# Optimization experiments

Hardware: AMD Instinct MI355X
Metric: run time of the kernel (lower is better)

## Reference

```python
import jax, jax.numpy as jnp
import numpy as np

TAU = 2.0        # LIFNode tau
ALPHA = 4.0      # spikingjelly default Sigmoid surrogate alpha
SCALE = 0.125    # attention scale from SSA
EPS = 1e-5       # BatchNorm eps

@jax.custom_vjp
def heaviside(x):
    return (x >= 0).astype(x.dtype)

def _hv_fwd(x):
    return (x >= 0).astype(x.dtype), x

def _hv_bwd(x, g):
    s = jax.nn.sigmoid(ALPHA * x)
    return (g * ALPHA * s * (1.0 - s),)

heaviside.defvjp(_hv_fwd, _hv_bwd)

def lif(x_seq, v_th):
    """Multi-step LIF (decay_input=True, v_reset=0, hard reset, detach_reset=True).
    x_seq: (T, ...) -> spikes (T, ...)."""
    def step(v, x):
        h = v + (x - v) / TAU                      # membrane charge
        s = heaviside(h - v_th)                    # spike
        v_new = h * (1.0 - jax.lax.stop_gradient(s))  # detached hard reset to 0
        return v_new, s
    _, spikes = jax.lax.scan(step, jnp.zeros_like(x_seq[0]), x_seq)
    return spikes

def conv_bn(x, w, gamma, beta, mean, var):
    """3x3 same-pad conv (no bias) + BatchNorm2d (eval: running stats), applied over merged T*B."""
    T, B, C, H, W = x.shape
    y = jax.lax.conv_general_dilated(
        x.reshape(T * B, C, H, W), w, (1, 1), 'SAME',
        dimension_numbers=('NCHW', 'OIHW', 'NCHW'))
    scale = gamma / jnp.sqrt(var + EPS)
    y = y * scale[:, None, None] + (beta - mean * scale)[:, None, None]
    return y.reshape(T, B, C, H, W)

def setup_inputs() -> dict:
    key = jax.random.key(0)
    T, B, C, H, W = 4, 16, 768, 16, 16
    ks = jax.random.split(key, 5)
    d = {"x": jax.random.normal(ks[0], (T, B, C, H, W), jnp.float32)}
    for i, p in enumerate(["q", "k", "v", "p"]):
        kk = jax.random.split(ks[i + 1], 5)
        d[p + "_w"] = jax.random.normal(kk[0], (C, C, 3, 3), jnp.float32) * 0.02
        d[p + "_gamma"] = jax.random.uniform(kk[1], (C,), jnp.float32, 0.5, 1.5)
        d[p + "_beta"] = jax.random.normal(kk[2], (C,), jnp.float32) * 0.1
        d[p + "_mean"] = jax.random.normal(kk[3], (C,), jnp.float32) * 0.1
        d[p + "_var"] = jax.random.uniform(kk[4], (C,), jnp.float32, 0.5, 1.5)
    return d

def reference(x, q_w, q_gamma, q_beta, q_mean, q_var,
              k_w, k_gamma, k_beta, k_mean, k_var,
              v_w, v_gamma, v_beta, v_mean, v_var,
              p_w, p_gamma, p_beta, p_mean, p_var):
    T, B, C, H, W = x.shape
    N = H * W
    nh = 8
    dh = C // nh
    xs = lif(x, 1.0)                                   # head_lif
    # Scaler is identity in eval mode (and rate=1.0)
    q = lif(conv_bn(xs, q_w, q_gamma, q_beta, q_mean, q_var), 1.0)
    k = lif(conv_bn(xs, k_w, k_gamma, k_beta, k_mean, k_var), 1.0)
    v = lif(conv_bn(xs, v_w, v_gamma, v_beta, v_mean, v_var), 1.0)
    def to_heads(t):  # (T,B,C,H,W) -> (T,B,nh,N,dh)
        return t.reshape(T, B, C, N).transpose(0, 1, 3, 2).reshape(T, B, N, nh, dh).transpose(0, 1, 3, 2, 4)
    q, k, v = to_heads(q), to_heads(k), to_heads(v)
    kv = jnp.einsum('tbhnd,tbhne->tbhde', k, v)        # k^T @ v (linear attention)
    o = jnp.einsum('tbhnd,tbhde->tbhne', q, kv) * SCALE
    o = o.transpose(0, 1, 2, 4, 3).reshape(T, B, C, N)  # (T,B,h,d,N) -> (T,B,C,N)
    o = lif(o, 0.5).reshape(T, B, C, H, W)              # attn_lif with v_threshold=0.5
    return conv_bn(o, p_w, p_gamma, p_beta, p_mean, p_var)
```

## Files before the change

### kernel.cpp

```cpp
#include <hip/hip_runtime.h>

typedef __attribute__((ext_vector_type(4))) int   i32x4;
typedef __attribute__((ext_vector_type(4))) float f32x4;
typedef unsigned int u32;
typedef unsigned long long u64;
typedef unsigned char u8;
typedef unsigned short u16;

#define C_ 768
#define NPIX 256
#define ROWB 96
#define IMGBITS (324*ROWB)
#define GS   304
#define PRS  1232
#define AEXP_SZ 12320

#define WFRAG_SZ 10616832ull
#define OFF_WFRAG 0ull
#define OFF_WCOL  31850496ull
#define OFF_YBUF  42467328ull
#define OFF_BITS  92798976ull
#define BITSZ     1990656ull
#define OFF_SBT   102752256ull
#define OFF_WMAX  102776832ull

__device__ __forceinline__ i32x4 as_i4(uint4 v){ union{uint4 u; i32x4 s;} c; c.u=v; return c.s; }
#define SPREAD(NIB) ((u32)__mul24((int)(NIB), 0x204081) & 0x01010101u)

__global__ __launch_bounds__(256) void bn_prep4(
    const float* __restrict__ g0, const float* __restrict__ b0,
    const float* __restrict__ m0, const float* __restrict__ v0,
    const float* __restrict__ g1, const float* __restrict__ b1,
    const float* __restrict__ m1, const float* __restrict__ v1,
    const float* __restrict__ g2, const float* __restrict__ b2,
    const float* __restrict__ m2, const float* __restrict__ v2,
    const float* __restrict__ g3, const float* __restrict__ b3,
    const float* __restrict__ m3, const float* __restrict__ v3,
    float* __restrict__ out)
{
    int s = blockIdx.y;
    const float* g  = s==0?g0:s==1?g1:s==2?g2:g3;
    const float* be = s==0?b0:s==1?b1:s==2?b2:b3;
    const float* m  = s==0?m0:s==1?m1:s==2?m2:m3;
    const float* va = s==0?v0:s==1?v1:s==2?v2:v3;
    int i = blockIdx.x*256 + threadIdx.x;
    if (i < C_){
        float sc = g[i] / sqrtf(va[i] + 1e-5f);
        out[s*1536 + i] = sc;
        out[s*1536 + C_ + i] = be[i] - m[i]*sc;
    }
}

__global__ __launch_bounds__(256) void wmax4(
    const float* __restrict__ w0, const float* __restrict__ w1,
    const float* __restrict__ w2, const float* __restrict__ w3,
    float* __restrict__ out)
{
    int s = blockIdx.y;
    const float* w = s==0?w0:s==1?w1:s==2?w2:w3;
    const int n4 = 9*C_*C_/4;
    float m = 0.f;
    for (int i = blockIdx.x*256 + threadIdx.x; i < n4; i += 65536){
        f32x4 v = *(const f32x4*)(w + (size_t)i*4);
        m = fmaxf(m, fmaxf(fmaxf(fabsf(v[0]), fabsf(v[1])),
                           fmaxf(fabsf(v[2]), fabsf(v[3]))));
    }
    #pragma unroll
    for (int off = 32; off >= 1; off >>= 1)
        m = fmaxf(m, __shfl_xor(m, off));
    if ((threadIdx.x & 63) == 0)
        atomicMax((int*)(out + s), __float_as_int(m));
}

__global__ __launch_bounds__(256) void wprep_stage(
    const float* __restrict__ w0, const float* __restrict__ w1,
    const float* __restrict__ w2, const float* __restrict__ w3,
    const float* __restrict__ wmaxb, u8* __restrict__ wfbase,
    short* __restrict__ wcol)
{
    __shared__ float lds[16][580];
    const int tid = threadIdx.x;
    const int nfg = blockIdx.x, cch = blockIdx.y, s = blockIdx.z;
    const float* w = s==0?w0:s==1?w1:s==2?w2:w3;
    const float mw = wmaxb[s];
    const float invS = (mw > 0.f) ? (32512.0f / mw) : 0.f;

    #pragma unroll 1
    for (int i = tid; i < 16*144; i += 256){
        int r = i / 144, f4 = i - r*144;
        f32x4 v = *(const f32x4*)(w + (size_t)(nfg*16 + r)*6912 + cch*576 + f4*4);
        *(f32x4*)&lds[r][f4*4] = v;
    }
    __syncthreads();

    if (s < 3){
        u8* wf = wfbase + (size_t)s*WFRAG_SZ;
        #pragma unroll 1
        for (int rep = 0; rep < 3; ++rep){
            int idx = rep*256 + tid;
            if (idx < 576){
                int tap = idx >> 6, lane = idx & 63;
                int co_r = lane & 15, cg = lane >> 4;
                u32 hw[4] = {0,0,0,0}, lw[4] = {0,0,0,0};
                #pragma unroll
                for (int e=0;e<16;++e){
                    float f = lds[co_r][(cg*16 + e)*9 + tap];
                    int w16 = __float2int_rn(f * invS);
                    w16 = min(max(w16, -32512), 32512);
                    int hi = (w16 + 128) >> 8;
                    int lo = w16 - (hi << 8);
                    hw[e>>2] |= ((u32)(hi & 0xFF)) << ((e&3)*8);
                    lw[e>>2] |= ((u32)(lo & 0xFF)) << ((e&3)*8);
                }
                u8* base = wf + (((size_t)(cch*9 + tap)*48 + nfg)*2)*1024 + (size_t)lane*16;
                *(uint4*)(base)        = make_uint4(hw[0],hw[1],hw[2],hw[3]);
                *(uint4*)(base + 1024) = make_uint4(lw[0],lw[1],lw[2],lw[3]);
            }
        }
    } else {
        #pragma unroll 1
        for (int rep = 0; rep < 3; ++rep){
            int idx = rep*256 + tid;
            if (idx < 576){
                int tap = idx >> 6, cl = idx & 63;
                short ov[16];
                #pragma unroll
                for (int r=0;r<16;++r){
                    float f = lds[r][cl*9 + tap];
                    int w16 = __float2int_rn(f * invS);
                    w16 = min(max(w16, -32512), 32512);
                    ov[r] = (short)w16;
                }
                short* dst = wcol + ((size_t)tap*C_ + cch*64 + cl)*C_ + nfg*16;
                *(uint4*)(dst)     = *(uint4*)(&ov[0]);
                *(uint4*)(dst + 8) = *(uint4*)(&ov[8]);
            }
        }
    }
}

__global__ __launch_bounds__(256) void head_bits(
    const float* __restrict__ x, u8* __restrict__ bits)
{
    int gid = blockIdx.x*256 + threadIdx.x;
    int b = gid / 24576, rem = gid - b*24576;
    int cb = rem >> 8, pix = rem & 255;
    int pr = ((pix>>4)+1)*18 + (pix&15) + 1;
    float v[8];
    #pragma unroll
    for (int j=0;j<8;++j) v[j]=0.f;
    #pragma unroll
    for (int t=0;t<4;++t){
        int img = t*16 + b;
        u32 byte = 0;
        #pragma unroll
        for (int j=0;j<8;++j){
            float xv = x[((size_t)img*C_ + cb*8 + j)*NPIX + pix];
            float h = __fadd_rn(v[j], __fmul_rn(__fsub_rn(xv, v[j]), 0.5f));
            u32 s = (h >= 1.0f) ? 1u : 0u;
            v[j] = s ? 0.f : h;
            byte |= s << j;
        }
        bits[(size_t)img*IMGBITS + (size_t)pr*ROWB + cb] = (u8)byte;
    }
}

__global__ __launch_bounds__(256,2) void conv_i8(
    const u8* __restrict__ abits, const u8* __restrict__ wf,
    const float* __restrict__ sb, const float* __restrict__ wmaxp,
    float* __restrict__ ybuf)
{
    __shared__ __align__(16) u8 Aexp[2*AEXP_SZ];
    const int tid = threadIdx.x;
    const int bid = blockIdx.x;
    const int cox = bid & 7, mh = (bid >> 3) & 1, img = bid >> 4;
    const int lane = tid & 63, w = tid >> 6;
    const int wr = w >> 1, wc = w & 1;
    const int lrow = lane & 15, lgrp = lane >> 4;

    const int erow = (tid < 180) ? tid : 179;
    const int epr = erow / 18, epc = erow - epr*18;
    u8* edst = Aexp + epr*PRS + epc*16;
    const u8* bsrc = abits + (size_t)img*IMGBITS + (size_t)(mh*144)*ROWB;

#define EXPW(BW, BOFF) if (tid < 180){ \
    u8* dp = edst + (BOFF); \
    u32 lo_ = (u32)(BW), hi_ = (u32)((BW)>>32); \
    *(uint4*)(dp       ) = make_uint4(SPREAD(lo_&0xF), SPREAD((lo_>>4)&0xF), SPREAD((lo_>>8)&0xF), SPREAD((lo_>>12)&0xF)); \
    *(uint4*)(dp + GS  ) = make_uint4(SPREAD((lo_>>16)&0xF), SPREAD((lo_>>20)&0xF), SPREAD((lo_>>24)&0xF), SPREAD((lo_>>28)&0xF)); \
    *(uint4*)(dp + 2*GS) = make_uint4(SPREAD(hi_&0xF), SPREAD((hi_>>4)&0xF), SPREAD((hi_>>8)&0xF), SPREAD((hi_>>12)&0xF)); \
    *(uint4*)(dp + 3*GS) = make_uint4(SPREAD((hi_>>16)&0xF), SPREAD((hi_>>20)&0xF), SPREAD((hi_>>24)&0xF), SPREAD((hi_>>28)&0xF)); }

    const u8* wp = wf + (size_t)((cox*6 + wc*3)*2)*1024 + (size_t)lane*16;
    uint4 R0[6], R1[6], R2[6];
#define LOADB(BUF) { \
    _Pragma("unroll") \
    for (int j=0;j<6;++j) BUF[j] = *(const uint4*)(wp + (j>>1)*2048 + (j&1)*1024); \
    wp += 98304; }

    int rb[4];
    #pragma unroll
    for (int mi=0;mi<4;++mi)
        rb[mi] = (wr*4 + mi + 1)*PRS + lgrp*GS + (lrow+1)*16;

    i32x4 acc_h[4][3], acc_l[4][3];
    #pragma unroll
    for (int mi=0;mi<4;++mi)
        #pragma unroll
        for (int ni=0;ni<3;++ni)
            #pragma unroll
            for (int r=0;r<4;++r){ acc_h[mi][ni][r]=0; acc_l[mi][ni][r]=0; }

#define COMPUTE(BUF, AE, TAP) { \
    const int DT = ((TAP)/3 - 1)*PRS + (((TAP)%3) - 1)*16; \
    i32x4 af[4]; \
    _Pragma("unroll") \
    for (int mi=0;mi<4;++mi) af[mi] = *(const i32x4*)((AE) + rb[mi] + DT); \
    __builtin_amdgcn_s_setprio(1); \
    _Pragma("unroll") \
    for (int mi=0;mi<4;++mi){ \
        _Pragma("unroll") \
        for (int ni=0;ni<3;++ni){ \
            acc_h[mi][ni] = __builtin_amdgcn_mfma_i32_16x16x64_i8(af[mi], as_i4(BUF[ni*2+0]), acc_h[mi][ni], 0,0,0); \
            acc_l[mi][ni] = __builtin_amdgcn_mfma_i32_16x16x64_i8(af[mi], as_i4(BUF[ni*2+1]), acc_l[mi][ni], 0,0,0); \
        } \
    } \
    __builtin_amdgcn_s_setprio(0); }

#define BODY(CCH, BOFF) { \
    u64 bwn = 0; \
    if ((CCH) < 11) bwn = *(const u64*)(bsrc + erow*ROWB + ((CCH)+1)*8); \
    const u8* Ae = Aexp + (BOFF); \
    LOADB(R2); COMPUTE(R0, Ae, 0); \
    LOADB(R0); COMPUTE(R1, Ae, 1); \
    LOADB(R1); COMPUTE(R2, Ae, 2); \
    LOADB(R2); COMPUTE(R0, Ae, 3); \
    LOADB(R0); COMPUTE(R1, Ae, 4); \
    LOADB(R1); COMPUTE(R2, Ae, 5); \
    LOADB(R2); COMPUTE(R0, Ae, 6); \
    LOADB(R0); COMPUTE(R1, Ae, 7); \
    LOADB(R1); COMPUTE(R2, Ae, 8); \
    if ((CCH) < 11) EXPW(bwn, (BOFF) ^ AEXP_SZ); \
    __syncthreads(); }

    LOADB(R0); LOADB(R1);
    {
        u64 bw0 = *(const u64*)(bsrc + erow*ROWB);
        EXPW(bw0, 0);
    }
    __syncthreads();

    #pragma unroll 1
    for (int c2=0; c2<6; ++c2){
        BODY(2*c2,   0);
        BODY(2*c2+1, AEXP_SZ);
    }
#undef LOADB
#undef EXPW
#undef COMPUTE
#undef BODY

    const float S = (*wmaxp) * (1.0f/32512.0f);
    #pragma unroll
    for (int mi=0;mi<4;++mi){
        const int prow = mh*128 + wr*64 + mi*16 + lgrp*4;
        #pragma unroll
        for (int ni=0;ni<3;++ni){
            const int co = cox*96 + wc*48 + ni*16 + lrow;
            const float sc = sb[co], bi = sb[C_ + co];
            #pragma unroll
            for (int r=0;r<4;++r){
                float accf = (float)(acc_h[mi][ni][r]*256 + acc_l[mi][ni][r]) * S;
                ybuf[((size_t)img*NPIX + prow + r)*C_ + co] =
                    __fadd_rn(__fmul_rn(accf, sc), bi);
            }
        }
    }
}

__global__ __launch_bounds__(256) void lif_bits(
    const float* __restrict__ y, u8* __restrict__ bits)
{
    int gid = blockIdx.x*256 + threadIdx.x;
    int b = gid / 24576, rem = gid - b*24576;
    int pix = rem / 96, cb = rem - pix*96;
    int pr = ((pix>>4)+1)*18 + (pix&15) + 1;
    float v[8];
    #pragma unroll
    for (int j=0;j<8;++j) v[j]=0.f;
    #pragma unroll
    for (int t=0;t<4;++t){
        int img = t*16 + b;
        const float* yp = y + ((size_t)img*NPIX + pix)*C_ + cb*8;
        f32x4 y0 = *(const f32x4*)yp;
        f32x4 y1 = *(const f32x4*)(yp + 4);
        u32 byte = 0;
        #pragma unroll
        for (int j=0;j<8;++j){
            float yv = (j<4) ? y0[j] : y1[j-4];
            float h = __fadd_rn(v[j], __fmul_rn(__fsub_rn(yv, v[j]), 0.5f));
            u32 s = (h >= 1.0f) ? 1u : 0u;
            v[j] = s ? 0.f : h;
            byte |= s << j;
        }
        bits[(size_t)img*IMGBITS + (size_t)pr*ROWB + cb] = (u8)byte;
    }
}

__global__ __launch_bounds__(512) void attn_bits(
    const u8* __restrict__ qb_, const u8* __restrict__ kb_,
    const u8* __restrict__ vb_, u8* __restrict__ ob)
{
    const int tid = threadIdx.x;
    const int b = blockIdx.x, h = blockIdx.y;
    __shared__ u64 kb[96][4], vb[96][4];
    __shared__ float kvl[96][96];
    const int w = tid >> 6, lane = tid & 63;
    const int ng = w & 3, n_build = ng*64 + lane;
    const int n = tid & 255, eh = tid >> 8;
    const int prb = ((n_build>>4)+1)*18 + (n_build&15) + 1;
    const int prn = ((n>>4)+1)*18 + (n&15) + 1;
    float vmem[48];
    #pragma unroll
    for (int e=0;e<48;++e) vmem[e]=0.f;

    for (int t=0;t<4;++t){
        const int img = t*16 + b;
        {
            const u8* src = (w < 4 ? kb_ : vb_) + (size_t)img*IMGBITS
                          + (size_t)prb*ROWB + h*12;
            u32 kw0 = ((const u32*)src)[0];
            u32 kw1 = ((const u32*)src)[1];
            u32 kw2 = ((const u32*)src)[2];
            u64 (*dst)[4] = (w < 4) ? kb : vb;
            #pragma unroll 1
            for (int dj=0; dj<32; ++dj){
                u64 m = __ballot((int)((kw0 >> dj) & 1u));
                if (lane == 0) dst[dj][ng] = m;
            }
            #pragma unroll 1
            for (int dj=0; dj<32; ++dj){
                u64 m = __ballot((int)((kw1 >> dj) & 1u));
                if (lane == 0) dst[32+dj][ng] = m;
            }
            #pragma unroll 1
            for (int dj=0; dj<32; ++dj){
                u64 m = __ballot((int)((kw2 >> dj) & 1u));
                if (lane == 0) dst[64+dj][ng] = m;
            }
        }
        __syncthreads();
        for (int i = tid; i < 96*96; i += 512){
            int d = i / 96, e = i - d*96;
            int s = 0;
            #pragma unroll
            for (int g=0; g<4; ++g) s += __popcll(kb[d][g] & vb[e][g]);
            kvl[d][e] = (float)s;
        }
        __syncthreads();
        {
            const u8* qsrc = qb_ + (size_t)img*IMGBITS + (size_t)prn*ROWB + h*12;
            u32 qw0 = ((const u32*)qsrc)[0];
            u32 qw1 = ((const u32*)qsrc)[1];
            u32 qw2 = ((const u32*)qsrc)[2];
            float val[48];
            #pragma unroll
            for (int e=0;e<48;++e) val[e]=0.f;
            #pragma unroll 1
            for (int d=0; d<96; ++d){
                u32 ww = (d < 32) ? qw0 : (d < 64) ? qw1 : qw2;
                u32 qv = (ww >> (d & 31)) & 1u;
                if (__any((int)qv)){
                    float qf = (float)qv;
                    #pragma unroll
                    for (int e=0;e<48;++e) val[e] += qf * kvl[d][eh*48+e];
                }
            }
            u64 wbits = 0;
            #pragma unroll
            for (int e=0;e<48;++e){
                float o = val[e]*0.125f;
                float hh = __fadd_rn(vmem[e], __fmul_rn(__fsub_rn(o, vmem[e]), 0.5f));
                u32 s = (hh >= 0.5f) ? 1u : 0u;
                vmem[e] = s ? 0.f : hh;
                wbits |= (u64)s << e;
            }
            u8* od = ob + (size_t)img*IMGBITS + (size_t)prn*ROWB + h*12 + eh*6;
            *(u16*)(od)     = (u16)(wbits);
            *(u16*)(od + 2) = (u16)(wbits >> 16);
            *(u16*)(od + 4) = (u16)(wbits >> 32);
        }
        __syncthreads();
    }
}

__global__ __launch_bounds__(256) void pconv_sparse(
    const u8* __restrict__ ob, const short* __restrict__ wcol,
    const float* __restrict__ sb, const float* __restrict__ wmaxp,
    float* __restrict__ out)
{
    __shared__ u64 bl[648];
    __shared__ int accL[16*768];
    const int tid = threadIdx.x;
    const int img = blockIdx.x >> 4, y = blockIdx.x & 15;

    for (int idx = tid; idx < 648; idx += 256){
        int d = idx / 216, wi = idx - d*216;
        bl[idx] = *(const u64*)(ob + (size_t)img*IMGBITS
                                + (size_t)((y+d)*18)*ROWB + (size_t)wi*8);
    }
    for (int idx = tid; idx < 16*768; idx += 256) accL[idx] = 0;
    __syncthreads();

    #pragma unroll 1
    for (int wi = 0; wi < 648; ++wi){
        u64 v = bl[wi];
        if (!v) continue;
        while (v){
            int j = __ffsll((unsigned long long)v) - 1;
            v &= v - 1;
            int byt = wi*8 + (j >> 3);
            int p = byt / 96;
            int c = (byt - p*96)*8 + (j & 7);
            int dd = p / 18, px = p - dd*18;
            #pragma unroll
            for (int xi = 0; xi < 3; ++xi){
                int x = px - 2 + xi;
                if ((unsigned)x < 16u){
                    int tap = dd*3 + 2 - xi;
                    const short* wr_ = wcol + ((size_t)tap*C_ + c)*C_;
                    #pragma unroll
                    for (int q = 0; q < 3; ++q){
                        int co = tid + q*256;
                        accL[x*768 + co] += (int)wr_[co];
                    }
                }
            }
        }
    }
    __syncthreads();

    const float S = wmaxp[0] * (1.0f/32512.0f);
    #pragma unroll
    for (int q = 0; q < 3; ++q){
        int co = tid + q*256;
        float sc = sb[co], bi = sb[C_ + co];
        float* op = out + ((size_t)img*C_ + co)*NPIX + y*16;
        #pragma unroll
        for (int xg = 0; xg < 4; ++xg){
            f32x4 o4;
            #pragma unroll
            for (int rr = 0; rr < 4; ++rr){
                float accf = (float)accL[(xg*4+rr)*768 + co] * S;
                o4[rr] = __fadd_rn(__fmul_rn(accf, sc), bi);
            }
            *(f32x4*)(op + xg*4) = o4;
        }
    }
}

extern "C" void kernel_launch(void* const* d_in, const int* in_sizes, int n_in,
                              void* d_out, int out_size, void* d_ws, size_t ws_size,
                              hipStream_t stream)
{
    u8* ws = (u8*)d_ws;
    u8* wfrag = ws + OFF_WFRAG;
    short* wcol = (short*)(ws + OFF_WCOL);
    float* ybuf = (float*)(ws + OFF_YBUF);
    u8* xs_b = ws + OFF_BITS;
    u8* q_b  = ws + OFF_BITS + 1*BITSZ;
    u8* k_b  = ws + OFF_BITS + 2*BITSZ;
    u8* v_b  = ws + OFF_BITS + 3*BITSZ;
    u8* o_b  = ws + OFF_BITS + 4*BITSZ;
    float* sbt = (float*)(ws + OFF_SBT);
    float* wmaxb = (float*)(ws + OFF_WMAX);
    float* outp = (float*)d_out;

    hipMemsetAsync(ws + OFF_BITS, 0, 5*BITSZ, stream);
    hipMemsetAsync(wmaxb, 0, 16, stream);

    bn_prep4<<<dim3(3,4),256,0,stream>>>(
        (const float*)d_in[2],  (const float*)d_in[3],  (const float*)d_in[4],  (const float*)d_in[5],
        (const float*)d_in[7],  (const float*)d_in[8],  (const float*)d_in[9],  (const float*)d_in[10],
        (const float*)d_in[12], (const float*)d_in[13], (const float*)d_in[14], (const float*)d_in[15],
        (const float*)d_in[17], (const float*)d_in[18], (const float*)d_in[19], (const float*)d_in[20],
        sbt);
    wmax4<<<dim3(256,4),256,0,stream>>>(
        (const float*)d_in[1], (const float*)d_in[6],
        (const float*)d_in[11], (const float*)d_in[16], wmaxb);
    wprep_stage<<<dim3(48,12,4),256,0,stream>>>(
        (const float*)d_in[1], (const float*)d_in[6],
        (const float*)d_in[11], (const float*)d_in[16], wmaxb, wfrag, wcol);
    head_bits<<<1536,256,0,stream>>>((const float*)d_in[0], xs_b);

    u8* bitp[3] = {q_b, k_b, v_b};
    for (int s=0;s<3;++s){
        conv_i8<<<1024,256,0,stream>>>(xs_b, wfrag + (size_t)s*WFRAG_SZ,
                                       sbt + s*1536, wmaxb + s, ybuf);
        lif_bits<<<1536,256,0,stream>>>(ybuf, bitp[s]);
    }
    attn_bits<<<dim3(16,8),512,0,stream>>>(q_b, k_b, v_b, o_b);
    pconv_sparse<<<1024,256,0,stream>>>(o_b, wcol, sbt + 4608, wmaxb + 3, outp);
}
```

Before: 602.4 us.

## Switch int8 conv MFMA from 16x16x64 to 32x32x32 tiles

Reworks the int8 conv kernel to use 32x32x32 MFMA instructions with 16-wide accumulators instead of 16x16x64. The weight fragment layout in the prep kernel is repacked to match, and each wave now owns 32 pixel rows across the full 96 output channels. The K dimension per tap is split into two halves, which doubles the number of pipeline steps. The aim is fewer LDS A-fragment reads per MFMA and better operand reuse per instruction, at the cost of a new register and load pattern and per-wave ownership of all 96 channels.

```diff
diff --git a/kernel.cpp b/kernel.cpp
--- a/kernel.cpp
+++ b/kernel.cpp
@@ -1,7 +1,8 @@
 #include <hip/hip_runtime.h>
 
-typedef __attribute__((ext_vector_type(4))) int   i32x4;
-typedef __attribute__((ext_vector_type(4))) float f32x4;
+typedef __attribute__((ext_vector_type(4)))  int   i32x4;
+typedef __attribute__((ext_vector_type(16))) int   i32x16;
+typedef __attribute__((ext_vector_type(4)))  float f32x4;
 typedef unsigned int u32;
 typedef unsigned long long u64;
 typedef unsigned char u8;
@@ -95,16 +96,18 @@
 
     if (s < 3){
         u8* wf = wfbase + (size_t)s*WFRAG_SZ;
+        const int nfg32 = nfg >> 1, h16 = nfg & 1;
         #pragma unroll 1
         for (int rep = 0; rep < 3; ++rep){
             int idx = rep*256 + tid;
             if (idx < 576){
-                int tap = idx >> 6, lane = idx & 63;
-                int co_r = lane & 15, cg = lane >> 4;
+                int co_r = idx & 15, kpart = (idx >> 4) & 1;
+                int kh = (idx >> 5) & 1, tap = idx >> 6;
                 u32 hw[4] = {0,0,0,0}, lw[4] = {0,0,0,0};
                 #pragma unroll
                 for (int e=0;e<16;++e){
-                    float f = lds[co_r][(cg*16 + e)*9 + tap];
+                    int cl = kh*32 + kpart*16 + e;
+                    float f = lds[co_r][cl*9 + tap];
                     int w16 = __float2int_rn(f * invS);
                     w16 = min(max(w16, -32512), 32512);
                     int hi = (w16 + 128) >> 8;
@@ -112,7 +115,9 @@
                     hw[e>>2] |= ((u32)(hi & 0xFF)) << ((e&3)*8);
                     lw[e>>2] |= ((u32)(lo & 0xFF)) << ((e&3)*8);
                 }
-                u8* base = wf + (((size_t)(cch*9 + tap)*48 + nfg)*2)*1024 + (size_t)lane*16;
+                int lane = kpart*32 + h16*16 + co_r;
+                u8* base = wf + ((((size_t)(cch*9 + tap)*2 + kh)*24 + nfg32)*2)*1024
+                              + (size_t)lane*16;
                 *(uint4*)(base)        = make_uint4(hw[0],hw[1],hw[2],hw[3]);
                 *(uint4*)(base + 1024) = make_uint4(lw[0],lw[1],lw[2],lw[3]);
             }
@@ -175,8 +180,7 @@
     const int bid = blockIdx.x;
     const int cox = bid & 7, mh = (bid >> 3) & 1, img = bid >> 4;
     const int lane = tid & 63, w = tid >> 6;
-    const int wr = w >> 1, wc = w & 1;
-    const int lrow = lane & 15, lgrp = lane >> 4;
+    const int l31 = lane & 31, kp = lane >> 5;
 
     const int erow = (tid < 180) ? tid : 179;
     const int epr = erow / 18, epc = erow - epr*18;
@@ -191,39 +195,29 @@
     *(uint4*)(dp + 2*GS) = make_uint4(SPREAD(hi_&0xF), SPREAD((hi_>>4)&0xF), SPREAD((hi_>>8)&0xF), SPREAD((hi_>>12)&0xF)); \
     *(uint4*)(dp + 3*GS) = make_uint4(SPREAD((hi_>>16)&0xF), SPREAD((hi_>>20)&0xF), SPREAD((hi_>>24)&0xF), SPREAD((hi_>>28)&0xF)); }
 
-    const u8* wp = wf + (size_t)((cox*6 + wc*3)*2)*1024 + (size_t)lane*16;
+    const u8* wp = wf + (size_t)(cox*3)*2048 + (size_t)lane*16;
     uint4 R0[6], R1[6], R2[6];
 #define LOADB(BUF) { \
     _Pragma("unroll") \
     for (int j=0;j<6;++j) BUF[j] = *(const uint4*)(wp + (j>>1)*2048 + (j&1)*1024); \
-    wp += 98304; }
-
-    int rb[4];
-    #pragma unroll
-    for (int mi=0;mi<4;++mi)
-        rb[mi] = (wr*4 + mi + 1)*PRS + lgrp*GS + (lrow+1)*16;
-
-    i32x4 acc_h[4][3], acc_l[4][3];
-    #pragma unroll
-    for (int mi=0;mi<4;++mi)
+    wp += 49152; }
+
+    const int rb = (w*2 + (l31>>4) + 1)*PRS + kp*GS + ((lane&15)+1)*16;
+
+    i32x16 acc_h[3], acc_l[3];
+    #pragma unroll
+    for (int ni=0;ni<3;++ni)
         #pragma unroll
-        for (int ni=0;ni<3;++ni)
-            #pragma unroll
-            for (int r=0;r<4;++r){ acc_h[mi][ni][r]=0; acc_l[mi][ni][r]=0; }
-
-#define COMPUTE(BUF, AE, TAP) { \
-    const int DT = ((TAP)/3 - 1)*PRS + (((TAP)%3) - 1)*16; \
-    i32x4 af[4]; \
-    _Pragma("unroll") \
-    for (int mi=0;mi<4;++mi) af[mi] = *(const i32x4*)((AE) + rb[mi] + DT); \
+        for (int r=0;r<16;++r){ acc_h[ni][r]=0; acc_l[ni][r]=0; }
+
+#define COMPUTE(BUF, AE, TAP, KH) { \
+    const int DT = ((TAP)/3 - 1)*PRS + (((TAP)%3) - 1)*16 + (KH)*(2*GS); \
+    i32x4 af = *(const i32x4*)((AE) + rb + DT); \
     __builtin_amdgcn_s_setprio(1); \
     _Pragma("unroll") \
-    for (int mi=0;mi<4;++mi){ \
-        _Pragma("unroll") \
-        for (int ni=0;ni<3;++ni){ \
-            acc_h[mi][ni] = __builtin_amdgcn_mfma_i32_16x16x64_i8(af[mi], as_i4(BUF[ni*2+0]), acc_h[mi][ni], 0,0,0); \
-            acc_l[mi][ni] = __builtin_amdgcn_mfma_i32_16x16x64_i8(af[mi], as_i4(BUF[ni*2+1]), acc_l[mi][ni], 0,0,0); \
-        } \
+    for (int ni=0;ni<3;++ni){ \
+        acc_h[ni] = __builtin_amdgcn_mfma_i32_32x32x32_i8(af, as_i4(BUF[ni*2+0]), acc_h[ni], 0,0,0); \
+        acc_l[ni] = __builtin_amdgcn_mfma_i32_32x32x32_i8(af, as_i4(BUF[ni*2+1]), acc_l[ni], 0,0,0); \
     } \
     __builtin_amdgcn_s_setprio(0); }
 
@@ -231,15 +225,24 @@
     u64 bwn = 0; \
     if ((CCH) < 11) bwn = *(const u64*)(bsrc + erow*ROWB + ((CCH)+1)*8); \
     const u8* Ae = Aexp + (BOFF); \
-    LOADB(R2); COMPUTE(R0, Ae, 0); \
-    LOADB(R0); COMPUTE(R1, Ae, 1); \
-    LOADB(R1); COMPUTE(R2, Ae, 2); \
-    LOADB(R2); COMPUTE(R0, Ae, 3); \
-    LOADB(R0); COMPUTE(R1, Ae, 4); \
-    LOADB(R1); COMPUTE(R2, Ae, 5); \
-    LOADB(R2); COMPUTE(R0, Ae, 6); \
-    LOADB(R0); COMPUTE(R1, Ae, 7); \
-    LOADB(R1); COMPUTE(R2, Ae, 8); \
+    LOADB(R2); COMPUTE(R0, Ae, 0,0); \
+    LOADB(R0); COMPUTE(R1, Ae, 0,1); \
+    LOADB(R1); COMPUTE(R2, Ae, 1,0); \
+    LOADB(R2); COMPUTE(R0, Ae, 1,1); \
+    LOADB(R0); COMPUTE(R1, Ae, 2,0); \
+    LOADB(R1); COMPUTE(R2, Ae, 2,1); \
+    LOADB(R2); COMPUTE(R0, Ae, 3,0); \
+    LOADB(R0); COMPUTE(R1, Ae, 3,1); \
+    LOADB(R1); COMPUTE(R2, Ae, 4,0); \
+    LOADB(R2); COMPUTE(R0, Ae, 4,1); \
+    LOADB(R0); COMPUTE(R1, Ae, 5,0); \
+    LOADB(R1); COMPUTE(R2, Ae, 5,1); \
+    LOADB(R2); COMPUTE(R0, Ae, 6,0); \
+    LOADB(R0); COMPUTE(R1, Ae, 6,1); \
+    LOADB(R1); COMPUTE(R2, Ae, 7,0); \
+    LOADB(R2); COMPUTE(R0, Ae, 7,1); \
+    LOADB(R0); COMPUTE(R1, Ae, 8,0); \
+    LOADB(R1); COMPUTE(R2, Ae, 8,1); \
     if ((CCH) < 11) EXPW(bwn, (BOFF) ^ AEXP_SZ); \
     __syncthreads(); }
 
@@ -262,18 +265,16 @@
 
     const float S = (*wmaxp) * (1.0f/32512.0f);
     #pragma unroll
-    for (int mi=0;mi<4;++mi){
-        const int prow = mh*128 + wr*64 + mi*16 + lgrp*4;
+    for (int ni=0;ni<3;++ni){
+        const int co = cox*96 + ni*32 + l31;
+        const float sc = sb[co], bi = sb[C_ + co];
         #pragma unroll
-        for (int ni=0;ni<3;++ni){
-            const int co = cox*96 + wc*48 + ni*16 + lrow;
-            const float sc = sb[co], bi = sb[C_ + co];
-            #pragma unroll
-            for (int r=0;r<4;++r){
-                float accf = (float)(acc_h[mi][ni][r]*256 + acc_l[mi][ni][r]) * S;
-                ybuf[((size_t)img*NPIX + prow + r)*C_ + co] =
-                    __fadd_rn(__fmul_rn(accf, sc), bi);
-            }
+        for (int r=0;r<16;++r){
+            const int row = (r & 3) + 8*(r >> 2) + 4*kp;
+            const int pix = mh*128 + w*32 + row;
+            float accf = (float)(acc_h[ni][r]*256 + acc_l[ni][r]) * S;
+            ybuf[((size_t)img*NPIX + pix)*C_ + co] =
+                __fadd_rn(__fmul_rn(accf, sc), bi);
         }
     }
 }
```

After: 802.9 us. 33.3% more time.

## Fuse LIF into conv kernel by tiling all four timesteps per block

Applied to the files above, without the earlier changes.

The q/k/v conv kernel now assigns each block a batch index and a 32-pixel segment across all four timesteps, instead of one image and half its pixels. This lets the LIF recurrence run in registers in the epilogue, with spike bits packed through a wave ballot and written straight to the bit buffers. The float ybuf round trip and the separate lif_bits launches go away. In exchange the shared-memory expansion buffer grows to hold four timestep tiles, and each block covers fewer pixels per timestep, which changes the reuse of weight fragments.

```diff
diff --git a/kernel.cpp b/kernel.cpp
--- a/kernel.cpp
+++ b/kernel.cpp
@@ -13,16 +13,16 @@
 #define IMGBITS (324*ROWB)
 #define GS   304
 #define PRS  1232
-#define AEXP_SZ 12320
+#define TPL  4928
+#define AEXP2 19712
 
 #define WFRAG_SZ 10616832ull
 #define OFF_WFRAG 0ull
 #define OFF_WCOL  31850496ull
-#define OFF_YBUF  42467328ull
-#define OFF_BITS  92798976ull
+#define OFF_BITS  42467328ull
 #define BITSZ     1990656ull
-#define OFF_SBT   102752256ull
-#define OFF_WMAX  102776832ull
+#define OFF_SBT   52420608ull
+#define OFF_WMAX  52445184ull
 
 __device__ __forceinline__ i32x4 as_i4(uint4 v){ union{uint4 u; i32x4 s;} c; c.u=v; return c.s; }
 #define SPREAD(NIB) ((u32)__mul24((int)(NIB), 0x204081) & 0x01010101u)
@@ -165,31 +165,37 @@
     }
 }
 
-__global__ __launch_bounds__(256,2) void conv_i8(
+__global__ __launch_bounds__(256,2) void conv_lif(
     const u8* __restrict__ abits, const u8* __restrict__ wf,
     const float* __restrict__ sb, const float* __restrict__ wmaxp,
-    float* __restrict__ ybuf)
-{
-    __shared__ __align__(16) u8 Aexp[2*AEXP_SZ];
+    u8* __restrict__ obits)
+{
+    __shared__ __align__(16) u8 Aexp[2*AEXP2];
     const int tid = threadIdx.x;
     const int bid = blockIdx.x;
-    const int cox = bid & 7, mh = (bid >> 3) & 1, img = bid >> 4;
+    const int cox = bid & 7, mseg = (bid >> 3) & 7, bq = bid >> 6;
     const int lane = tid & 63, w = tid >> 6;
     const int wr = w >> 1, wc = w & 1;
     const int lrow = lane & 15, lgrp = lane >> 4;
 
-    const int erow = (tid < 180) ? tid : 179;
-    const int epr = erow / 18, epc = erow - epr*18;
-    u8* edst = Aexp + epr*PRS + epc*16;
-    const u8* bsrc = abits + (size_t)img*IMGBITS + (size_t)(mh*144)*ROWB;
-
-#define EXPW(BW, BOFF) if (tid < 180){ \
-    u8* dp = edst + (BOFF); \
+    const int t0u = tid / 72, p0 = tid - t0u*72;
+    const int epr0 = p0 / 18, epc0 = p0 - epr0*18;
+    const u8* b0 = abits + (size_t)(t0u*16 + bq)*IMGBITS
+                 + (size_t)((mseg*2 + epr0)*18 + epc0)*ROWB;
+    const int d0off = t0u*TPL + epr0*PRS + epc0*16;
+    const bool has2 = (tid < 32);
+    const int p1 = tid + 40;
+    const int epr1 = p1 / 18, epc1 = p1 - epr1*18;
+    const u8* b1 = abits + (size_t)(3*16 + bq)*IMGBITS
+                 + (size_t)((mseg*2 + epr1)*18 + epc1)*ROWB;
+    const int d1off = 3*TPL + epr1*PRS + epc1*16;
+
+#define EXPW(BW, DP){ \
     u32 lo_ = (u32)(BW), hi_ = (u32)((BW)>>32); \
-    *(uint4*)(dp       ) = make_uint4(SPREAD(lo_&0xF), SPREAD((lo_>>4)&0xF), SPREAD((lo_>>8)&0xF), SPREAD((lo_>>12)&0xF)); \
-    *(uint4*)(dp + GS  ) = make_uint4(SPREAD((lo_>>16)&0xF), SPREAD((lo_>>20)&0xF), SPREAD((lo_>>24)&0xF), SPREAD((lo_>>28)&0xF)); \
-    *(uint4*)(dp + 2*GS) = make_uint4(SPREAD(hi_&0xF), SPREAD((hi_>>4)&0xF), SPREAD((hi_>>8)&0xF), SPREAD((hi_>>12)&0xF)); \
-    *(uint4*)(dp + 3*GS) = make_uint4(SPREAD((hi_>>16)&0xF), SPREAD((hi_>>20)&0xF), SPREAD((hi_>>24)&0xF), SPREAD((hi_>>28)&0xF)); }
+    *(uint4*)((DP)       ) = make_uint4(SPREAD(lo_&0xF), SPREAD((lo_>>4)&0xF), SPREAD((lo_>>8)&0xF), SPREAD((lo_>>12)&0xF)); \
+    *(uint4*)((DP) + GS  ) = make_uint4(SPREAD((lo_>>16)&0xF), SPREAD((lo_>>20)&0xF), SPREAD((lo_>>24)&0xF), SPREAD((lo_>>28)&0xF)); \
+    *(uint4*)((DP) + 2*GS) = make_uint4(SPREAD(hi_&0xF), SPREAD((hi_>>4)&0xF), SPREAD((hi_>>8)&0xF), SPREAD((hi_>>12)&0xF)); \
+    *(uint4*)((DP) + 3*GS) = make_uint4(SPREAD((hi_>>16)&0xF), SPREAD((hi_>>20)&0xF), SPREAD((hi_>>24)&0xF), SPREAD((hi_>>28)&0xF)); }
 
     const u8* wp = wf + (size_t)((cox*6 + wc*3)*2)*1024 + (size_t)lane*16;
     uint4 R0[6], R1[6], R2[6];
@@ -198,38 +204,36 @@
     for (int j=0;j<6;++j) BUF[j] = *(const uint4*)(wp + (j>>1)*2048 + (j&1)*1024); \
     wp += 98304; }
 
-    int rb[4];
-    #pragma unroll
-    for (int mi=0;mi<4;++mi)
-        rb[mi] = (wr*4 + mi + 1)*PRS + lgrp*GS + (lrow+1)*16;
+    const int rb = (wr + 1)*PRS + lgrp*GS + (lrow + 1)*16;
 
     i32x4 acc_h[4][3], acc_l[4][3];
     #pragma unroll
-    for (int mi=0;mi<4;++mi)
+    for (int t=0;t<4;++t)
         #pragma unroll
         for (int ni=0;ni<3;++ni)
             #pragma unroll
-            for (int r=0;r<4;++r){ acc_h[mi][ni][r]=0; acc_l[mi][ni][r]=0; }
+            for (int r=0;r<4;++r){ acc_h[t][ni][r]=0; acc_l[t][ni][r]=0; }
 
 #define COMPUTE(BUF, AE, TAP) { \
     const int DT = ((TAP)/3 - 1)*PRS + (((TAP)%3) - 1)*16; \
-    i32x4 af[4]; \
     _Pragma("unroll") \
-    for (int mi=0;mi<4;++mi) af[mi] = *(const i32x4*)((AE) + rb[mi] + DT); \
-    __builtin_amdgcn_s_setprio(1); \
-    _Pragma("unroll") \
-    for (int mi=0;mi<4;++mi){ \
+    for (int t=0;t<4;++t){ \
+        i32x4 af = *(const i32x4*)((AE) + t*TPL + rb + DT); \
+        __builtin_amdgcn_s_setprio(1); \
         _Pragma("unroll") \
         for (int ni=0;ni<3;++ni){ \
-            acc_h[mi][ni] = __builtin_amdgcn_mfma_i32_16x16x64_i8(af[mi], as_i4(BUF[ni*2+0]), acc_h[mi][ni], 0,0,0); \
-            acc_l[mi][ni] = __builtin_amdgcn_mfma_i32_16x16x64_i8(af[mi], as_i4(BUF[ni*2+1]), acc_l[mi][ni], 0,0,0); \
+            acc_h[t][ni] = __builtin_amdgcn_mfma_i32_16x16x64_i8(af, as_i4(BUF[ni*2+0]), acc_h[t][ni], 0,0,0); \
+            acc_l[t][ni] = __builtin_amdgcn_mfma_i32_16x16x64_i8(af, as_i4(BUF[ni*2+1]), acc_l[t][ni], 0,0,0); \
         } \
+        __builtin_amdgcn_s_setprio(0); \
+    } }
+
+#define BODY(CCH, BOFF) { \
+    u64 bw0n = 0, bw1n = 0; \
+    if ((CCH) < 11){ \
+        bw0n = *(const u64*)(b0 + ((CCH)+1)*8); \
+        if (has2) bw1n = *(const u64*)(b1 + ((CCH)+1)*8); \
     } \
-    __builtin_amdgcn_s_setprio(0); }
-
-#define BODY(CCH, BOFF) { \
-    u64 bwn = 0; \
-    if ((CCH) < 11) bwn = *(const u64*)(bsrc + erow*ROWB + ((CCH)+1)*8); \
     const u8* Ae = Aexp + (BOFF); \
     LOADB(R2); COMPUTE(R0, Ae, 0); \
     LOADB(R0); COMPUTE(R1, Ae, 1); \
@@ -240,20 +244,27 @@
     LOADB(R2); COMPUTE(R0, Ae, 6); \
     LOADB(R0); COMPUTE(R1, Ae, 7); \
     LOADB(R1); COMPUTE(R2, Ae, 8); \
-    if ((CCH) < 11) EXPW(bwn, (BOFF) ^ AEXP_SZ); \
+    if ((CCH) < 11){ \
+        EXPW(bw0n, Aexp + ((BOFF) ^ AEXP2) + d0off); \
+        if (has2) EXPW(bw1n, Aexp + ((BOFF) ^ AEXP2) + d1off); \
+    } \
     __syncthreads(); }
 
     LOADB(R0); LOADB(R1);
     {
-        u64 bw0 = *(const u64*)(bsrc + erow*ROWB);
-        EXPW(bw0, 0);
+        u64 bw0 = *(const u64*)(b0);
+        EXPW(bw0, Aexp + d0off);
+        if (has2){
+            u64 bw1 = *(const u64*)(b1);
+            EXPW(bw1, Aexp + d1off);
+        }
     }
     __syncthreads();
 
     #pragma unroll 1
     for (int c2=0; c2<6; ++c2){
         BODY(2*c2,   0);
-        BODY(2*c2+1, AEXP_SZ);
+        BODY(2*c2+1, AEXP2);
     }
 #undef LOADB
 #undef EXPW
@@ -261,49 +272,42 @@
 #undef BODY
 
     const float S = (*wmaxp) * (1.0f/32512.0f);
-    #pragma unroll
-    for (int mi=0;mi<4;++mi){
-        const int prow = mh*128 + wr*64 + mi*16 + lgrp*4;
+    float scs[3], bis[3];
+    #pragma unroll
+    for (int ni=0;ni<3;++ni){
+        const int co = cox*96 + wc*48 + ni*16 + lrow;
+        scs[ni] = sb[co]; bis[ni] = sb[C_ + co];
+    }
+    float vmem[3][4];
+    #pragma unroll
+    for (int ni=0;ni<3;++ni)
+        #pragma unroll
+        for (int r=0;r<4;++r) vmem[ni][r] = 0.f;
+
+    const int pixb = mseg*32 + wr*16 + lgrp*4;
+    const int prn0 = ((pixb>>4)+1)*18 + (pixb&15) + 1;
+    #pragma unroll
+    for (int t=0;t<4;++t){
+        const size_t ibase = (size_t)(t*16 + bq)*IMGBITS;
         #pragma unroll
         for (int ni=0;ni<3;++ni){
-            const int co = cox*96 + wc*48 + ni*16 + lrow;
-            const float sc = sb[co], bi = sb[C_ + co];
             #pragma unroll
             for (int r=0;r<4;++r){
-                float accf = (float)(acc_h[mi][ni][r]*256 + acc_l[mi][ni][r]) * S;
-                ybuf[((size_t)img*NPIX + prow + r)*C_ + co] =
-                    __fadd_rn(__fmul_rn(accf, sc), bi);
-            }
-        }
-    }
-}
-
-__global__ __launch_bounds__(256) void lif_bits(
-    const float* __restrict__ y, u8* __restrict__ bits)
-{
-    int gid = blockIdx.x*256 + threadIdx.x;
-    int b = gid / 24576, rem = gid - b*24576;
-    int pix = rem / 96, cb = rem - pix*96;
-    int pr = ((pix>>4)+1)*18 + (pix&15) + 1;
-    float v[8];
-    #pragma unroll
-    for (int j=0;j<8;++j) v[j]=0.f;
-    #pragma unroll
-    for (int t=0;t<4;++t){
-        int img = t*16 + b;
-        const float* yp = y + ((size_t)img*NPIX + pix)*C_ + cb*8;
-        f32x4 y0 = *(const f32x4*)yp;
-        f32x4 y1 = *(const f32x4*)(yp + 4);
-        u32 byte = 0;
-        #pragma unroll
-        for (int j=0;j<8;++j){
-            float yv = (j<4) ? y0[j] : y1[j-4];
-            float h = __fadd_rn(v[j], __fmul_rn(__fsub_rn(yv, v[j]), 0.5f));
-            u32 s = (h >= 1.0f) ? 1u : 0u;
-            v[j] = s ? 0.f : h;
-            byte |= s << j;
-        }
-        bits[(size_t)img*IMGBITS + (size_t)pr*ROWB + cb] = (u8)byte;
+                int sum = acc_h[t][ni][r]*256 + acc_l[t][ni][r];
+                float accf = (float)sum * S;
+                float y = __fadd_rn(__fmul_rn(accf, scs[ni]), bis[ni]);
+                float h = __fadd_rn(vmem[ni][r],
+                          __fmul_rn(__fsub_rn(y, vmem[ni][r]), 0.5f));
+                u32 s = (h >= 1.0f) ? 1u : 0u;
+                vmem[ni][r] = s ? 0.f : h;
+                u64 mask = __ballot((int)s);
+                if (lrow == 0){
+                    u16 fld = (u16)(mask >> (lgrp*16));
+                    *(u16*)(obits + ibase + (size_t)(prn0 + r)*ROWB
+                            + cox*12 + wc*6 + ni*2) = fld;
+                }
+            }
+        }
     }
 }
 
@@ -466,7 +470,6 @@
     u8* ws = (u8*)d_ws;
     u8* wfrag = ws + OFF_WFRAG;
     short* wcol = (short*)(ws + OFF_WCOL);
-    float* ybuf = (float*)(ws + OFF_YBUF);
     u8* xs_b = ws + OFF_BITS;
     u8* q_b  = ws + OFF_BITS + 1*BITSZ;
     u8* k_b  = ws + OFF_BITS + 2*BITSZ;
@@ -495,9 +498,8 @@
 
     u8* bitp[3] = {q_b, k_b, v_b};
     for (int s=0;s<3;++s){
-        conv_i8<<<1024,256,0,stream>>>(xs_b, wfrag + (size_t)s*WFRAG_SZ,
-                                       sbt + s*1536, wmaxb + s, ybuf);
-        lif_bits<<<1536,256,0,stream>>>(ybuf, bitp[s]);
+        conv_lif<<<1024,256,0,stream>>>(xs_b, wfrag + (size_t)s*WFRAG_SZ,
+                                        sbt + s*1536, wmaxb + s, bitp[s]);
     }
     attn_bits<<<dim3(16,8),512,0,stream>>>(q_b, k_b, v_b, o_b);
     pconv_sparse<<<1024,256,0,stream>>>(o_b, wcol, sbt + 4608, wmaxb + 3, outp);
```

Result: no change. 610.1 us (+1.3%).
